# Optimization experiments

Hardware: AMD Instinct MI355X
Metric: run time of the kernel (lower is better)

The kernel has to match this reference:

```python
import jax, jax.numpy as jnp
import numpy as np

V = 50000        # fine nodes
E = 400000       # edges
NEXT_DIM = 12500 # coarse nodes (nextDim)
B = 2
FIN, FOUT = 64, 128


def setup_inputs() -> dict:
    key = jax.random.key(0)
    ks = jax.random.split(key, 12)
    x = jax.random.normal(ks[0], (B, V, FIN), dtype=jnp.float32)
    adjValue = jax.random.uniform(ks[1], (E,), dtype=jnp.float32)
    edgeOne = jnp.ones((E,), dtype=jnp.float32)
    E_start = jax.random.randint(ks[2], (E,), 0, V, dtype=jnp.int32)
    E_end = jax.random.randint(ks[3], (E,), 0, V, dtype=jnp.int32)
    # avg-pool assignment: each fine node v -> coarse node v//4, weight 1/4
    fine = jnp.arange(V, dtype=jnp.int32)
    avgPoolAsgnIdx = jnp.stack([fine // 4, fine])  # [2, nnz]
    avgPoolAsgnValue = jnp.full((V,), 0.25, dtype=jnp.float32)
    s = 0.05
    W_res = jax.random.normal(ks[4], (FIN, FOUT), dtype=jnp.float32) * s
    b_res = jnp.zeros((FOUT,), dtype=jnp.float32)
    W0_self = jax.random.normal(ks[5], (FIN, FOUT), dtype=jnp.float32) * s
    W0_nb = jax.random.normal(ks[6], (FIN, FOUT), dtype=jnp.float32) * s
    b0 = jnp.zeros((FOUT,), dtype=jnp.float32)
    W1_self = jax.random.normal(ks[7], (FOUT, FOUT), dtype=jnp.float32) * s
    W1_nb = jax.random.normal(ks[8], (FOUT, FOUT), dtype=jnp.float32) * s
    b1 = jnp.zeros((FOUT,), dtype=jnp.float32)
    return {"x": x, "adjValue": adjValue, "edgeOne": edgeOne,
            "E_start": E_start, "E_end": E_end,
            "avgPoolAsgnIdx": avgPoolAsgnIdx, "avgPoolAsgnValue": avgPoolAsgnValue,
            "W_res": W_res, "b_res": b_res,
            "W0_self": W0_self, "W0_nb": W0_nb, "b0": b0,
            "W1_self": W1_self, "W1_nb": W1_nb, "b1": b1}


def _ecc(x, Ws, Wn, b, adjValue, E_start, E_end, deg_inv):
    # Edge-conditioned conv: out_i = x_i Ws + (1/deg_i) * sum_{e: start=i} adj_e * (x_{end(e)} Wn) + b
    Bn, Vn, _ = x.shape
    h = jnp.einsum('bvf,fo->bvo', x, Wn)            # neighbor transform [B,V,Fo]
    ht = h.transpose(1, 0, 2).reshape(Vn, -1)       # [V, B*Fo]
    msg = ht[E_end] * adjValue[:, None]             # gather + edge weight [E, B*Fo]
    agg = jax.ops.segment_sum(msg, E_start, num_segments=Vn)  # scatter-add [V, B*Fo]
    agg = (agg * deg_inv[:, None]).reshape(Vn, Bn, -1).transpose(1, 0, 2)
    return jnp.einsum('bvf,fo->bvo', x, Ws) + agg + b


def _batch_spmm(idx, value, m, x):
    # sparse (m x n) @ x per batch; x: [B, n, F]
    Bn, n, F = x.shape
    xt = x.transpose(1, 0, 2).reshape(n, -1)        # [n, B*F]
    g = xt[idx[1]] * value[:, None]                 # [nnz, B*F]
    out = jax.ops.segment_sum(g, idx[0], num_segments=m)
    return out.reshape(m, Bn, F).transpose(1, 0, 2)


def reference(x, adjValue, edgeOne, E_start, E_end, avgPoolAsgnIdx, avgPoolAsgnValue,
              W_res, b_res, W0_self, W0_nb, b0, W1_self, W1_nb, b1):
    deg = jax.ops.segment_sum(edgeOne, E_start, num_segments=V)
    deg_inv = 1.0 / jnp.maximum(deg, 1.0)
    # residual path: 1x1 conv == per-node linear, then pool
    residual = jnp.einsum('bvf,fo->bvo', x, W_res) + b_res
    residual = _batch_spmm(avgPoolAsgnIdx, avgPoolAsgnValue, NEXT_DIM, residual)
    # main path: ECC -> leaky_relu(0.2) -> ECC -> pool
    out = _ecc(x, W0_self, W0_nb, b0, adjValue, E_start, E_end, deg_inv)
    out = jnp.where(out >= 0, out, 0.2 * out)
    out = _ecc(out, W1_self, W1_nb, b1, adjValue, E_start, E_end, deg_inv)
    out = _batch_spmm(avgPoolAsgnIdx, avgPoolAsgnValue, NEXT_DIM, out)
    return out + residual
```

## Files before the change

### kernel.cpp

```cpp
#include <hip/hip_runtime.h>

#define V_N    50000
#define E_N    400000
#define NEXT_N 12500
#define B_N    2
#define M_ROWS (V_N * B_N)
#define NSBLK  196

typedef float  f32x2  __attribute__((ext_vector_type(2)));
typedef float  f32x4  __attribute__((ext_vector_type(4)));
typedef __bf16 bf16x8 __attribute__((ext_vector_type(8)));
typedef int    i32x2  __attribute__((ext_vector_type(2)));
typedef unsigned int u32x2 __attribute__((ext_vector_type(2)));
typedef unsigned int u32x4 __attribute__((ext_vector_type(4)));

__device__ __forceinline__ float bflo(unsigned int u) {
    return __builtin_bit_cast(float, u << 16);
}
__device__ __forceinline__ float bfhi(unsigned int u) {
    return __builtin_bit_cast(float, u & 0xffff0000u);
}
__device__ __forceinline__ unsigned short bf16bits(float f) {
    return __builtin_bit_cast(unsigned short, (__bf16)f);
}

__device__ __forceinline__ void wcvt_one(int idx, int phase,
                                         const float* Wa, const float* Wb, const float* Wc,
                                         unsigned int* dst) {
    int kc = idx >> 11;
    int jj = idx & 3, lane = (idx >> 2) & 63, nt = (idx >> 8) & 7;
    int kk = kc * 32 + ((lane >> 4) * 8) + jj * 2;
    int n  = nt * 16 + (lane & 15);
    const float* Wsrc; int kbase;
    if (phase == 0) {
        if (kk < 64) { Wsrc = Wa; kbase = 0; } else { Wsrc = Wb; kbase = 64; }
    } else {
        if (kk < 128)      { Wsrc = Wa; kbase = 0; }
        else if (kk < 256) { Wsrc = Wb; kbase = 128; }
        else               { Wsrc = Wc; kbase = 256; }
    }
    float w0 = Wsrc[(kk - kbase) * 128 + n];
    float w1 = Wsrc[(kk + 1 - kbase) * 128 + n];
    dst[idx] = ((unsigned int)bf16bits(w1) << 16) | bf16bits(w0);
}

__global__ void prep_kernel(const float* __restrict__ x, unsigned int* __restrict__ xbf,
                            const int* __restrict__ Es, int* __restrict__ degi,
                            const int* __restrict__ poolIdx, const float* __restrict__ poolVal,
                            int* __restrict__ invRow, float* __restrict__ invVal,
                            const float* __restrict__ W0s, const float* __restrict__ W0n,
                            const float* __restrict__ W1s, const float* __restrict__ W1n,
                            const float* __restrict__ Wres,
                            unsigned int* __restrict__ Wc0, unsigned int* __restrict__ Wc1) {
    int blk = blockIdx.x, t = threadIdx.x;
    if (blk < 12500) {
        int i = blk * 256 + t;
        f32x2 p = *(const f32x2*)(x + (size_t)i * 2);
        xbf[i] = ((unsigned int)bf16bits(p[1]) << 16) | bf16bits(p[0]);
    } else if (blk < 14063) {
        int e = (blk - 12500) * 256 + t;
        if (e < E_N) atomicAdd(&degi[Es[e]], 1);
    } else if (blk < 14259) {
        int j = (blk - 14063) * 256 + t;
        if (j < V_N) {
            int c = poolIdx[V_N + j];
            invRow[c] = poolIdx[j];
            invVal[c] = poolVal[j];
        }
    } else if (blk < 14291) {
        wcvt_one((blk - 14259) * 256 + t, 0, W0s, W0n, nullptr, Wc0);
    } else {
        wcvt_one((blk - 14291) * 256 + t, 1, W1s, W1n, Wres, Wc1);
    }
}

__global__ __launch_bounds__(256) void scan_kernel(const int* __restrict__ degi,
                                                   int* __restrict__ counter,
                                                   int* __restrict__ aggP,
                                                   int* __restrict__ cur,
                                                   float* __restrict__ dinv) {
    __shared__ int sh[256];
    __shared__ int pref[256];
    __shared__ int shrank;
    int t = threadIdx.x;
    if (t == 0) shrank = atomicAdd(counter, 1);
    __syncthreads();
    int rank = shrank;
    int i = rank * 256 + t;
    int d = (i < V_N) ? degi[i] : 0;
    sh[t] = d;
    __syncthreads();
    for (int off = 1; off < 256; off <<= 1) {
        int v = (t >= off) ? sh[t - off] : 0;
        __syncthreads();
        sh[t] += v;
        __syncthreads();
    }
    int incl = sh[t];
    int blocksum = sh[255];
    if (t == 0)
        __hip_atomic_store(&aggP[rank], blocksum + 1, __ATOMIC_RELEASE,
                           __HIP_MEMORY_SCOPE_AGENT);
    int pv = 0;
    if (t < rank) {
        int v;
        do {
            v = __hip_atomic_load(&aggP[t], __ATOMIC_ACQUIRE, __HIP_MEMORY_SCOPE_AGENT);
        } while (v == 0);
        pv = v - 1;
    }
    pref[t] = pv;
    __syncthreads();
    for (int off = 128; off > 0; off >>= 1) {
        if (t < off) pref[t] += pref[t + off];
        __syncthreads();
    }
    int prefix = pref[0];
    if (i < V_N) {
        cur[i] = prefix + incl - d;
        dinv[i] = 1.0f / (float)(d > 1 ? d : 1);
    }
}

__global__ void csr_kernel(const int* __restrict__ Es, const int* __restrict__ Ee,
                           const float* __restrict__ adj, int* __restrict__ cur,
                           i32x2* __restrict__ ecv) {
    int e0 = (blockIdx.x * 256 + threadIdx.x) * 2;
    if (e0 >= E_N) return;
    i32x2 s2 = *(const i32x2*)(Es + e0);
    i32x2 d2 = *(const i32x2*)(Ee + e0);
    f32x2 a2 = *(const f32x2*)(adj + e0);
    {
        int pos = atomicAdd(&cur[s2[0]], 1);
        i32x2 p; p[0] = d2[0]; p[1] = __float_as_int(a2[0]);
        ecv[pos] = p;
    }
    {
        int pos = atomicAdd(&cur[s2[1]], 1);
        i32x2 p; p[0] = d2[1]; p[1] = __float_as_int(a2[1]);
        ecv[pos] = p;
    }
}

__global__ __launch_bounds__(256) void agg0_kernel(
    const unsigned int* __restrict__ xbf, const int* __restrict__ cur,
    const i32x2* __restrict__ ecv, const float* __restrict__ dinv,
    unsigned int* __restrict__ AGG0bf) {
    int w = blockIdx.x * 4 + (threadIdx.x >> 6);
    int lane = threadIdx.x & 63;
    int beg = w ? cur[w - 1] : 0;
    int end = cur[w];
    int b = lane >> 5, u = lane & 31;
    const unsigned int* src = xbf + (size_t)b * V_N * 32 + u;
    float s0 = 0.f, s1 = 0.f;
    for (int base = beg; base < end; base += 32) {
        int li = base + lane;
        bool lv = (lane < 32) && (li < end);
        i32x2 ev = lv ? ecv[li] : i32x2{0, 0};
        int dk = ev[0];
        float ak = lv ? __int_as_float(ev[1]) : 0.0f;
        int nrem = end - base; if (nrem > 32) nrem = 32;
        for (int jb = 0; jb < nrem; jb += 8) {
            unsigned int pv[8]; float av8[8];
#pragma unroll
            for (int j = 0; j < 8; ++j) {
                int dj = __shfl(dk, jb + j);
                av8[j] = __shfl(ak, jb + j);
                pv[j] = src[(size_t)dj * 32];
            }
#pragma unroll
            for (int j = 0; j < 8; ++j) { s0 += av8[j] * bflo(pv[j]); s1 += av8[j] * bfhi(pv[j]); }
        }
    }
    float dv = dinv[w];
    AGG0bf[((size_t)b * V_N + w) * 32 + u] =
        ((unsigned int)bf16bits(s1 * dv) << 16) | bf16bits(s0 * dv);
}

__global__ __launch_bounds__(256) void agg1_kernel(
    const unsigned int* __restrict__ obf, const int* __restrict__ cur,
    const i32x2* __restrict__ ecv, const float* __restrict__ dinv,
    unsigned int* __restrict__ AGG1bf) {
    int w = blockIdx.x * 4 + (threadIdx.x >> 6);
    int lane = threadIdx.x & 63;
    int beg = w ? cur[w - 1] : 0;
    int end = cur[w];
    int b = lane >> 5;
    int u = (lane & 31) * 2;
    const unsigned int* src = obf + (size_t)b * V_N * 64 + u;
    float s[4] = {0, 0, 0, 0};
    for (int base = beg; base < end; base += 32) {
        int li = base + lane;
        bool lv = (lane < 32) && (li < end);
        i32x2 ev = lv ? ecv[li] : i32x2{0, 0};
        int dk = ev[0];
        float ak = lv ? __int_as_float(ev[1]) : 0.0f;
        int nrem = end - base; if (nrem > 32) nrem = 32;
        for (int jb = 0; jb < nrem; jb += 8) {
            u32x2 pv[8]; float av8[8];
#pragma unroll
            for (int j = 0; j < 8; ++j) {
                int dj = __shfl(dk, jb + j);
                av8[j] = __shfl(ak, jb + j);
                pv[j] = *(const u32x2*)(src + (size_t)dj * 64);
            }
#pragma unroll
            for (int j = 0; j < 8; ++j) {
                s[0] += av8[j] * bflo(pv[j][0]); s[1] += av8[j] * bfhi(pv[j][0]);
                s[2] += av8[j] * bflo(pv[j][1]); s[3] += av8[j] * bfhi(pv[j][1]);
            }
        }
    }
    float dv = dinv[w];
    u32x2 r;
    r[0] = ((unsigned int)bf16bits(s[1] * dv) << 16) | bf16bits(s[0] * dv);
    r[1] = ((unsigned int)bf16bits(s[3] * dv) << 16) | bf16bits(s[2] * dv);
    *(u32x2*)(AGG1bf + ((size_t)b * V_N + w) * 64 + u) = r;
}

template <int PHASE>
__global__ __launch_bounds__(256) void gemm_kernel(
    const unsigned int* __restrict__ xbf, const unsigned int* __restrict__ INbf,
    const unsigned int* __restrict__ AGGbf, const unsigned int* __restrict__ Wcvt,
    const float* __restrict__ bias0, const float* __restrict__ bias1,
    const int* __restrict__ invRow, const float* __restrict__ invVal,
    unsigned short* __restrict__ OUTbf, float* __restrict__ out) {
    constexpr int K  = (PHASE == 0) ? 128 : 320;
    constexpr int KC = K / 32;

    __shared__ unsigned int ldsW[KC * 2048];

    const int tid  = threadIdx.x;
    const int wave = tid >> 6, lane = tid & 63;
    const int m = lane & 15, quad = lane >> 4;

    {
        const u32x4* src4 = (const u32x4*)Wcvt;
        u32x4* dst4 = (u32x4*)ldsW;
#pragma unroll
        for (int it = 0; it < 2 * KC; ++it) dst4[it * 256 + tid] = src4[it * 256 + tid];
    }
    __syncthreads();

    const int rowBase = blockIdx.x * 128 + wave * 32;
    int rA[2];
#pragma unroll
    for (int mt = 0; mt < 2; ++mt) {
        int r = rowBase + mt * 16 + m;
        rA[mt] = r < M_ROWS ? r : M_ROWS - 1;
    }

    f32x4 acc[2][8];
#pragma unroll
    for (int mt = 0; mt < 2; ++mt)
#pragma unroll
        for (int i = 0; i < 8; ++i)
#pragma unroll
            for (int r = 0; r < 4; ++r) acc[mt][i][r] = 0.0f;

#pragma unroll
    for (int kc = 0; kc < KC; ++kc) {
        int k0 = kc * 32 + quad * 8;
        bf16x8 av[2];
#pragma unroll
        for (int mt = 0; mt < 2; ++mt) {
            const unsigned int* abase;
            if (PHASE == 0) {
                abase = (k0 < 64) ? xbf + (size_t)rA[mt] * 32 + (k0 >> 1)
                                  : AGGbf + (size_t)rA[mt] * 32 + ((k0 - 64) >> 1);
            } else {
                if (k0 < 128)      abase = INbf + (size_t)rA[mt] * 64 + (k0 >> 1);
                else if (k0 < 256) abase = AGGbf + (size_t)rA[mt] * 64 + ((k0 - 128) >> 1);
                else               abase = xbf + (size_t)rA[mt] * 32 + ((k0 - 256) >> 1);
            }
            av[mt] = __builtin_bit_cast(bf16x8, *(const u32x4*)abase);
        }
#pragma unroll
        for (int nt = 0; nt < 8; ++nt) {
            bf16x8 bv = __builtin_bit_cast(
                bf16x8, *(const u32x4*)&ldsW[(kc * 8 + nt) * 256 + lane * 4]);
            acc[0][nt] = __builtin_amdgcn_mfma_f32_16x16x32_bf16(av[0], bv, acc[0][nt], 0, 0, 0);
            acc[1][nt] = __builtin_amdgcn_mfma_f32_16x16x32_bf16(av[1], bv, acc[1][nt], 0, 0, 0);
        }
    }

#pragma unroll
    for (int mt = 0; mt < 2; ++mt) {
        const int rowq = rowBase + mt * 16 + quad * 4;
        if (PHASE == 0) {
#pragma unroll
            for (int nt = 0; nt < 8; ++nt) {
                int o = nt * 16 + m;
                float bias = bias0[o];
#pragma unroll
                for (int r = 0; r < 4; ++r) {
                    int orow = rowq + r;
                    if (orow < M_ROWS) {
                        float val = acc[mt][nt][r] + bias;
                        val = val >= 0.0f ? val : 0.2f * val;
                        OUTbf[(size_t)orow * 128 + o] = bf16bits(val);
                    }
                }
            }
        } else {
            int b = rowq >= V_N;
            int vq = rowq - b * V_N;
            int rr0 = -2, rr1 = -2, rr2 = -2, rr3 = -2;
            float w0 = 0, w1 = 0, w2 = 0, w3 = 0;
            bool inb = (rowq + 3) < M_ROWS;
            if (inb) {
                rr0 = invRow[vq];     w0 = invVal[vq];
                rr1 = invRow[vq + 1]; w1 = invVal[vq + 1];
                rr2 = invRow[vq + 2]; w2 = invVal[vq + 2];
                rr3 = invRow[vq + 3]; w3 = invVal[vq + 3];
            }
            bool uniform = inb && (rr0 >= 0) && (rr0 == rr1) && (rr0 == rr2) && (rr0 == rr3);
#pragma unroll
            for (int nt = 0; nt < 8; ++nt) {
                int o = nt * 16 + m;
                float bias = bias0[o] + bias1[o];
                if (uniform) {
                    float pooled = w0 * (acc[mt][nt][0] + bias) + w1 * (acc[mt][nt][1] + bias) +
                                   w2 * (acc[mt][nt][2] + bias) + w3 * (acc[mt][nt][3] + bias);
                    out[((size_t)b * NEXT_N + rr0) * 128 + o] = pooled;
                } else {
#pragma unroll
                    for (int r = 0; r < 4; ++r) {
                        int orow = rowq + r;
                        if (orow < M_ROWS) {
                            int bb = orow >= V_N;
                            int vf = orow - bb * V_N;
                            int rrr = invRow[vf];
                            float www = invVal[vf];
                            if (rrr >= 0)
                                unsafeAtomicAdd(&out[((size_t)bb * NEXT_N + rrr) * 128 + o],
                                                www * (acc[mt][nt][r] + bias));
                        }
                    }
                }
            }
        }
    }
}


extern "C" void kernel_launch(void* const* d_in, const int* in_sizes, int n_in,
                              void* d_out, int out_size, void* d_ws, size_t ws_size,
                              hipStream_t stream) {
    const float* x       = (const float*)d_in[0];
    const float* adj     = (const float*)d_in[1];
    const int*   Es      = (const int*)d_in[3];
    const int*   Ee      = (const int*)d_in[4];
    const int*   poolIdx = (const int*)d_in[5];
    const float* poolVal = (const float*)d_in[6];
    const float* W_res   = (const float*)d_in[7];
    const float* b_res   = (const float*)d_in[8];
    const float* W0s     = (const float*)d_in[9];
    const float* W0n     = (const float*)d_in[10];
    const float* b0      = (const float*)d_in[11];
    const float* W1s     = (const float*)d_in[12];
    const float* W1n     = (const float*)d_in[13];
    const float* b1      = (const float*)d_in[14];
    float* out = (float*)d_out;

    char* ws = (char*)d_ws;
    int*   invRow  = (int*)  (ws + 0);
    float* invVal  = (float*)(ws + 200704);
    int*   degi    = (int*)  (ws + 401408);
    int*   counter = (int*)  (ws + 601408);
    int*   aggP    = (int*)  (ws + 601412);
    float* dinv    = (float*)(ws + 602624);
    int*   cur     = (int*)  (ws + 803328);
    i32x2* ecv     = (i32x2*)(ws + 1003520);
    unsigned int* Wc0 = (unsigned int*)(ws + 4203520);
    unsigned int* Wc1 = (unsigned int*)(ws + 4236288);
    unsigned int* xbf    = (unsigned int*)(ws + 4318208);
    unsigned int* AGG0bf = (unsigned int*)(ws + 17118208);
    unsigned int* OUT0bf = (unsigned int*)(ws + 29918208);
    unsigned int* AGG1bf = (unsigned int*)(ws + 55518208);

    (void)hipMemsetAsync(degi, 0, 200788, stream);

    prep_kernel<<<14371, 256, 0, stream>>>(x, xbf, Es, degi, poolIdx, poolVal,
                                           invRow, invVal, W0s, W0n, W1s, W1n, W_res,
                                           Wc0, Wc1);
    scan_kernel<<<NSBLK, 256, 0, stream>>>(degi, counter, aggP, cur, dinv);
    csr_kernel<<<(E_N / 2 + 255) / 256, 256, 0, stream>>>(Es, Ee, adj, cur, ecv);

    agg0_kernel<<<12500, 256, 0, stream>>>(xbf, cur, ecv, dinv, AGG0bf);
    gemm_kernel<0><<<(M_ROWS + 127) / 128, 256, 0, stream>>>(
        xbf, nullptr, AGG0bf, Wc0, b0, nullptr, invRow, invVal,
        (unsigned short*)OUT0bf, nullptr);
    agg1_kernel<<<12500, 256, 0, stream>>>(OUT0bf, cur, ecv, dinv, AGG1bf);
    gemm_kernel<1><<<(M_ROWS + 127) / 128, 256, 0, stream>>>(
        xbf, OUT0bf, AGG1bf, Wc1, b1, b_res, invRow, invVal,
        nullptr, out);
}
```

Baseline: 249.9 us.

## Restructure GEMM kernels to 512 threads, one M-tile per wave, split N in phase 1

Each wave now computes a single 16-row M tile instead of two, and blocks grow to 512 threads so each block still covers 128 rows. Phase 1 also splits the 128 output columns into two halves across separate blocks, halving the LDS weight footprint and the accumulator count per thread. The aim is lower register and LDS pressure, higher occupancy and more parallelism for latency hiding. In exchange, each weight fragment read from LDS feeds half as many MFMAs, and in phase 1 the A operand rows are loaded twice, once per column half.

```diff
diff --git a/kernel.cpp b/kernel.cpp
--- a/kernel.cpp
+++ b/kernel.cpp
@@ -6,6 +6,7 @@
 #define B_N    2
 #define M_ROWS (V_N * B_N)
 #define NSBLK  196
+#define NRT    782
 
 typedef float  f32x2  __attribute__((ext_vector_type(2)));
 typedef float  f32x4  __attribute__((ext_vector_type(4)));
@@ -219,7 +220,7 @@
 }
 
 template <int PHASE>
-__global__ __launch_bounds__(256) void gemm_kernel(
+__global__ __launch_bounds__(512) void gemm_kernel(
     const unsigned int* __restrict__ xbf, const unsigned int* __restrict__ INbf,
     const unsigned int* __restrict__ AGGbf, const unsigned int* __restrict__ Wcvt,
     const float* __restrict__ bias0, const float* __restrict__ bias1,
@@ -227,115 +228,106 @@
     unsigned short* __restrict__ OUTbf, float* __restrict__ out) {
     constexpr int K  = (PHASE == 0) ? 128 : 320;
     constexpr int KC = K / 32;
-
-    __shared__ unsigned int ldsW[KC * 2048];
+    constexpr int NT = (PHASE == 0) ? 8 : 4;
+
+    __shared__ unsigned int ldsW[KC * NT * 256];
 
     const int tid  = threadIdx.x;
     const int wave = tid >> 6, lane = tid & 63;
     const int m = lane & 15, quad = lane >> 4;
+    const int h = (PHASE == 1 && blockIdx.x >= NRT) ? 1 : 0;
+    const int rowtile = blockIdx.x - h * NRT;
 
     {
         const u32x4* src4 = (const u32x4*)Wcvt;
         u32x4* dst4 = (u32x4*)ldsW;
-#pragma unroll
-        for (int it = 0; it < 2 * KC; ++it) dst4[it * 256 + tid] = src4[it * 256 + tid];
+        for (int e = tid; e < KC * NT * 64; e += 512) {
+            int kcl = e / (NT * 64);
+            int rem = e - kcl * (NT * 64);
+            dst4[e] = src4[(kcl * 8 + h * NT) * 64 + rem];
+        }
     }
     __syncthreads();
 
-    const int rowBase = blockIdx.x * 128 + wave * 32;
-    int rA[2];
-#pragma unroll
-    for (int mt = 0; mt < 2; ++mt) {
-        int r = rowBase + mt * 16 + m;
-        rA[mt] = r < M_ROWS ? r : M_ROWS - 1;
-    }
-
-    f32x4 acc[2][8];
-#pragma unroll
-    for (int mt = 0; mt < 2; ++mt)
-#pragma unroll
-        for (int i = 0; i < 8; ++i)
-#pragma unroll
-            for (int r = 0; r < 4; ++r) acc[mt][i][r] = 0.0f;
+    const int rowA0 = rowtile * 128 + wave * 16 + m;
+    const int rA = rowA0 < M_ROWS ? rowA0 : M_ROWS - 1;
+
+    f32x4 acc[NT];
+#pragma unroll
+    for (int i = 0; i < NT; ++i)
+#pragma unroll
+        for (int r = 0; r < 4; ++r) acc[i][r] = 0.0f;
 
 #pragma unroll
     for (int kc = 0; kc < KC; ++kc) {
         int k0 = kc * 32 + quad * 8;
-        bf16x8 av[2];
-#pragma unroll
-        for (int mt = 0; mt < 2; ++mt) {
-            const unsigned int* abase;
-            if (PHASE == 0) {
-                abase = (k0 < 64) ? xbf + (size_t)rA[mt] * 32 + (k0 >> 1)
-                                  : AGGbf + (size_t)rA[mt] * 32 + ((k0 - 64) >> 1);
+        const unsigned int* abase;
+        if (PHASE == 0) {
+            abase = (k0 < 64) ? xbf + (size_t)rA * 32 + (k0 >> 1)
+                              : AGGbf + (size_t)rA * 32 + ((k0 - 64) >> 1);
+        } else {
+            if (k0 < 128)      abase = INbf + (size_t)rA * 64 + (k0 >> 1);
+            else if (k0 < 256) abase = AGGbf + (size_t)rA * 64 + ((k0 - 128) >> 1);
+            else               abase = xbf + (size_t)rA * 32 + ((k0 - 256) >> 1);
+        }
+        bf16x8 av = __builtin_bit_cast(bf16x8, *(const u32x4*)abase);
+#pragma unroll
+        for (int nt = 0; nt < NT; ++nt) {
+            bf16x8 bv = __builtin_bit_cast(
+                bf16x8, *(const u32x4*)&ldsW[(kc * NT + nt) * 256 + lane * 4]);
+            acc[nt] = __builtin_amdgcn_mfma_f32_16x16x32_bf16(av, bv, acc[nt], 0, 0, 0);
+        }
+    }
+
+    const int rowq = rowtile * 128 + wave * 16 + quad * 4;
+    if (PHASE == 0) {
+#pragma unroll
+        for (int nt = 0; nt < NT; ++nt) {
+            int o = nt * 16 + m;
+            float bias = bias0[o];
+#pragma unroll
+            for (int r = 0; r < 4; ++r) {
+                int orow = rowq + r;
+                if (orow < M_ROWS) {
+                    float val = acc[nt][r] + bias;
+                    val = val >= 0.0f ? val : 0.2f * val;
+                    OUTbf[(size_t)orow * 128 + o] = bf16bits(val);
+                }
+            }
+        }
+    } else {
+        int b = rowq >= V_N;
+        int vq = rowq - b * V_N;
+        int rr0 = -2, rr1 = -2, rr2 = -2, rr3 = -2;
+        float w0 = 0, w1 = 0, w2 = 0, w3 = 0;
+        bool inb = (rowq + 3) < M_ROWS;
+        if (inb) {
+            rr0 = invRow[vq];     w0 = invVal[vq];
+            rr1 = invRow[vq + 1]; w1 = invVal[vq + 1];
+            rr2 = invRow[vq + 2]; w2 = invVal[vq + 2];
+            rr3 = invRow[vq + 3]; w3 = invVal[vq + 3];
+        }
+        bool uniform = inb && (rr0 >= 0) && (rr0 == rr1) && (rr0 == rr2) && (rr0 == rr3);
+#pragma unroll
+        for (int nt = 0; nt < NT; ++nt) {
+            int o = h * 64 + nt * 16 + m;
+            float bias = bias0[o] + bias1[o];
+            if (uniform) {
+                float pooled = w0 * (acc[nt][0] + bias) + w1 * (acc[nt][1] + bias) +
+                               w2 * (acc[nt][2] + bias) + w3 * (acc[nt][3] + bias);
+                out[((size_t)b * NEXT_N + rr0) * 128 + o] = pooled;
             } else {
-                if (k0 < 128)      abase = INbf + (size_t)rA[mt] * 64 + (k0 >> 1);
-                else if (k0 < 256) abase = AGGbf + (size_t)rA[mt] * 64 + ((k0 - 128) >> 1);
-                else               abase = xbf + (size_t)rA[mt] * 32 + ((k0 - 256) >> 1);
-            }
-            av[mt] = __builtin_bit_cast(bf16x8, *(const u32x4*)abase);
-        }
-#pragma unroll
-        for (int nt = 0; nt < 8; ++nt) {
-            bf16x8 bv = __builtin_bit_cast(
-                bf16x8, *(const u32x4*)&ldsW[(kc * 8 + nt) * 256 + lane * 4]);
-            acc[0][nt] = __builtin_amdgcn_mfma_f32_16x16x32_bf16(av[0], bv, acc[0][nt], 0, 0, 0);
-            acc[1][nt] = __builtin_amdgcn_mfma_f32_16x16x32_bf16(av[1], bv, acc[1][nt], 0, 0, 0);
-        }
-    }
-
-#pragma unroll
-    for (int mt = 0; mt < 2; ++mt) {
-        const int rowq = rowBase + mt * 16 + quad * 4;
-        if (PHASE == 0) {
-#pragma unroll
-            for (int nt = 0; nt < 8; ++nt) {
-                int o = nt * 16 + m;
-                float bias = bias0[o];
 #pragma unroll
                 for (int r = 0; r < 4; ++r) {
                     int orow = rowq + r;
                     if (orow < M_ROWS) {
-                        float val = acc[mt][nt][r] + bias;
-                        val = val >= 0.0f ? val : 0.2f * val;
-                        OUTbf[(size_t)orow * 128 + o] = bf16bits(val);
-                    }
-                }
-            }
-        } else {
-            int b = rowq >= V_N;
-            int vq = rowq - b * V_N;
-            int rr0 = -2, rr1 = -2, rr2 = -2, rr3 = -2;
-            float w0 = 0, w1 = 0, w2 = 0, w3 = 0;
-            bool inb = (rowq + 3) < M_ROWS;
-            if (inb) {
-                rr0 = invRow[vq];     w0 = invVal[vq];
-                rr1 = invRow[vq + 1]; w1 = invVal[vq + 1];
-                rr2 = invRow[vq + 2]; w2 = invVal[vq + 2];
-                rr3 = invRow[vq + 3]; w3 = invVal[vq + 3];
-            }
-            bool uniform = inb && (rr0 >= 0) && (rr0 == rr1) && (rr0 == rr2) && (rr0 == rr3);
-#pragma unroll
-            for (int nt = 0; nt < 8; ++nt) {
-                int o = nt * 16 + m;
-                float bias = bias0[o] + bias1[o];
-                if (uniform) {
-                    float pooled = w0 * (acc[mt][nt][0] + bias) + w1 * (acc[mt][nt][1] + bias) +
-                                   w2 * (acc[mt][nt][2] + bias) + w3 * (acc[mt][nt][3] + bias);
-                    out[((size_t)b * NEXT_N + rr0) * 128 + o] = pooled;
-                } else {
-#pragma unroll
-                    for (int r = 0; r < 4; ++r) {
-                        int orow = rowq + r;
-                        if (orow < M_ROWS) {
-                            int bb = orow >= V_N;
-                            int vf = orow - bb * V_N;
-                            int rrr = invRow[vf];
-                            float www = invVal[vf];
-                            if (rrr >= 0)
-                                unsafeAtomicAdd(&out[((size_t)bb * NEXT_N + rrr) * 128 + o],
-                                                www * (acc[mt][nt][r] + bias));
-                        }
+                        int bb = orow >= V_N;
+                        int vf = orow - bb * V_N;
+                        int rrr = invRow[vf];
+                        float www = invVal[vf];
+                        if (rrr >= 0)
+                            unsafeAtomicAdd(&out[((size_t)bb * NEXT_N + rrr) * 128 + o],
+                                            www * (acc[nt][r] + bias));
                     }
                 }
             }
@@ -388,11 +380,11 @@
     csr_kernel<<<(E_N / 2 + 255) / 256, 256, 0, stream>>>(Es, Ee, adj, cur, ecv);
 
     agg0_kernel<<<12500, 256, 0, stream>>>(xbf, cur, ecv, dinv, AGG0bf);
-    gemm_kernel<0><<<(M_ROWS + 127) / 128, 256, 0, stream>>>(
+    gemm_kernel<0><<<NRT, 512, 0, stream>>>(
         xbf, nullptr, AGG0bf, Wc0, b0, nullptr, invRow, invVal,
         (unsigned short*)OUT0bf, nullptr);
     agg1_kernel<<<12500, 256, 0, stream>>>(OUT0bf, cur, ecv, dinv, AGG1bf);
-    gemm_kernel<1><<<(M_ROWS + 127) / 128, 256, 0, stream>>>(
+    gemm_kernel<1><<<2 * NRT, 512, 0, stream>>>(
         xbf, OUT0bf, AGG1bf, Wc1, b1, b_res, invRow, invVal,
         nullptr, out);
 }
```

Result: no change. 252.1 us (+0.9%).
